# Optimization experiments

Hardware: AMD Instinct MI355X
Metric: run time of the kernel (lower is better)

The kernel has to match this reference:

```python
import jax, jax.numpy as jnp
import numpy as np

BATCH = 4096
DIM = 128
TEMP = 0.5
EPS = 1e-8


def _neg_mask(batch):
    n = 2 * batch
    m = np.ones((n, n), dtype=bool)
    np.fill_diagonal(m, False)
    idx = np.arange(batch)
    m[idx, idx + batch] = False
    m[idx + batch, idx] = False
    return m


def setup_inputs() -> dict:
    key = jax.random.key(0)
    k1, k2 = jax.random.split(key)
    zx = jax.random.normal(k1, (BATCH, DIM), dtype=jnp.float32)
    zy = jax.random.normal(k2, (BATCH, DIM), dtype=jnp.float32)
    return {"zx": zx, "zy": zy}


def reference(zx, zy):
    batch = zx.shape[0]
    n = 2 * batch  # N = 2 * batch_size
    z = jnp.concatenate([zx, zy], axis=0)  # [N, D]
    # cosine similarity = normalized GEMM (avoids O(N^2*D) intermediate)
    norm = jnp.maximum(jnp.linalg.norm(z, axis=1, keepdims=True), EPS)
    zn = z / norm
    sim = (zn @ zn.T) / TEMP  # [N, N]
    # positives: diagonals at offsets +batch and -batch
    sim_xy = jnp.diagonal(sim, offset=batch)
    sim_yx = jnp.diagonal(sim, offset=-batch)
    positives = jnp.concatenate([sim_xy, sim_yx]).reshape(n, 1)  # [N, 1]
    # negatives: mask out diagonal and positive pairs (static boolean mask)
    mask = _neg_mask(batch)
    negatives = sim[mask].reshape(n, n - 2)  # [N, N-2]
    logits = jnp.concatenate([positives, negatives], axis=1)  # [N, N-1]
    # CrossEntropy(labels=0, reduction='sum') / N
    loss = jnp.sum(jax.nn.logsumexp(logits, axis=1) - logits[:, 0]) / n
    return loss
```

## Files before the change

kernel.cpp:

```cpp
#include <hip/hip_runtime.h>
#include <hip/hip_bf16.h>

#define BATCH 4096
#define NROWS 8192
#define DIM   128

typedef __bf16 bf16x8 __attribute__((ext_vector_type(8)));
typedef __bf16 bf16x2 __attribute__((ext_vector_type(2)));
typedef float  f32x4  __attribute__((ext_vector_type(4)));

typedef const __attribute__((address_space(1))) unsigned int* gptr_t;
typedef __attribute__((address_space(3))) unsigned int* lptr_t;

__global__ __launch_bounds__(256) void normalize_kernel(
    const float* __restrict__ zx, const float* __restrict__ zy,
    ushort* __restrict__ zn)
{
  const int tid  = threadIdx.x;
  const int lane = tid & 63;
  const int w    = tid >> 6;
  const int row  = blockIdx.x * 4 + w;
  const float* src = (row < BATCH) ? (zx + (size_t)row * DIM)
                                   : (zy + (size_t)(row - BATCH) * DIM);
  float2 v = ((const float2*)src)[lane];
  float ss = v.x * v.x + v.y * v.y;
#pragma unroll
  for (int off = 1; off < 64; off <<= 1)
    ss += __shfl_xor(ss, off, 64);
  float inv = 1.0f / fmaxf(sqrtf(ss), 1e-8f);
  bf16x2 st;
  st.x = (__bf16)(v.x * inv);
  st.y = (__bf16)(v.y * inv);
  reinterpret_cast<bf16x2*>(zn + (size_t)row * DIM)[lane] = st;
}

__global__ __launch_bounds__(256, 2) void simloss_kernel(
    const ushort* __restrict__ zn, float* __restrict__ S, float* __restrict__ P)
{
  __shared__ ushort Bs[128 * 128];
  const int tid  = threadIdx.x;
  const int lane = tid & 63;
  const int w    = tid >> 6;
  const int wr   = w >> 1, wc = w & 1;
  const int rb    = blockIdx.x;
  const int strip = blockIdx.y;
  const int q    = lane >> 4;
  const int l15  = lane & 15;

  bf16x8 af[4][4];
  {
    const int arow = rb * 128 + wr * 64 + l15;
#pragma unroll
    for (int mi = 0; mi < 4; ++mi)
#pragma unroll
      for (int ks = 0; ks < 4; ++ks) {
        const ushort* ap = zn + (size_t)(arow + mi * 16) * DIM + ks * 32 + q * 8;
        af[mi][ks] = *reinterpret_cast<const bf16x8*>(ap);
      }
  }

  float Srow[4][4];
#pragma unroll
  for (int mi = 0; mi < 4; ++mi)
#pragma unroll
    for (int r = 0; r < 4; ++r) Srow[mi][r] = 0.f;

  const float K1 = 2.8853900817779268f;

  for (int it = 0; it < 8; ++it) {
    const int ct = strip * 8 + it;
    const int C0 = ct * 128;

    __syncthreads();
#pragma unroll
    for (int j = 0; j < 8; ++j) {
      const int Lbase = w * 512 + j * 64;
      const int row   = w * 32 + j * 4 + q;
      const int c     = l15 ^ (row & 15);
      const ushort* g = zn + (size_t)(C0 + row) * DIM + c * 8;
      __builtin_amdgcn_global_load_lds((gptr_t)g, (lptr_t)(Bs + Lbase * 8), 16, 0, 0);
    }
    __syncthreads();

    f32x4 acc[4][4];
#pragma unroll
    for (int mi = 0; mi < 4; ++mi)
#pragma unroll
      for (int ni = 0; ni < 4; ++ni)
        acc[mi][ni] = (f32x4){0.f, 0.f, 0.f, 0.f};

#pragma unroll
    for (int ks = 0; ks < 4; ++ks) {
      bf16x8 bf[4];
#pragma unroll
      for (int ni = 0; ni < 4; ++ni) {
        const int nl  = wc * 64 + ni * 16 + l15;
        const int ck  = ks * 4 + q;
        const int L   = nl * 16 + (ck ^ (nl & 15));
        bf[ni] = *reinterpret_cast<const bf16x8*>(Bs + L * 8);
      }
#pragma unroll
      for (int mi = 0; mi < 4; ++mi)
#pragma unroll
        for (int ni = 0; ni < 4; ++ni)
          acc[mi][ni] = __builtin_amdgcn_mfma_f32_16x16x32_bf16(
              af[mi][ks], bf[ni], acc[mi][ni], 0, 0, 0);
    }

    const bool diag = (ct == rb);
    const bool part = (ct == (rb ^ 32));
#pragma unroll
    for (int mi = 0; mi < 4; ++mi)
#pragma unroll
      for (int ni = 0; ni < 4; ++ni)
#pragma unroll
        for (int r = 0; r < 4; ++r) {
          float d = acc[mi][ni][r];
          float v = __builtin_amdgcn_exp2f(fmaf(d, K1, -K1));
          if (diag) {
            const int rl = wr * 64 + mi * 16 + q * 4 + r;
            const int cl = wc * 64 + ni * 16 + l15;
            if (rl == cl) v = 0.f;
          }
          Srow[mi][r] += v;
        }

    if (part) {
#pragma unroll
      for (int mi = 0; mi < 4; ++mi) {
        const int rl0 = wr * 64 + mi * 16 + q * 4;
#pragma unroll
        for (int ni = 0; ni < 4; ++ni) {
          const int cl = wc * 64 + ni * 16 + l15;
#pragma unroll
          for (int r = 0; r < 4; ++r) {
            if (cl == rl0 + r)
              P[rb * 128 + rl0 + r] = 2.0f * acc[mi][ni][r];
          }
        }
      }
    }
  }

#pragma unroll
  for (int mi = 0; mi < 4; ++mi)
#pragma unroll
    for (int r = 0; r < 4; ++r) {
      float v = Srow[mi][r];
      v += __shfl_xor(v, 1, 64);
      v += __shfl_xor(v, 2, 64);
      v += __shfl_xor(v, 4, 64);
      v += __shfl_xor(v, 8, 64);
      if (l15 == 0)
        atomicAdd(&S[rb * 128 + wr * 64 + mi * 16 + q * 4 + r], v);
    }
}

__global__ __launch_bounds__(256) void finalize_kernel(
    const float* __restrict__ S, const float* __restrict__ P,
    float* __restrict__ out)
{
  const int i = blockIdx.x * 256 + threadIdx.x;
  float c = 2.0f + logf(S[i]) - P[i];
#pragma unroll
  for (int off = 1; off < 64; off <<= 1)
    c += __shfl_xor(c, off, 64);
  __shared__ float wsum[4];
  const int lane = threadIdx.x & 63, w = threadIdx.x >> 6;
  if (lane == 0) wsum[w] = c;
  __syncthreads();
  if (threadIdx.x == 0)
    atomicAdd(out, (wsum[0] + wsum[1] + wsum[2] + wsum[3]) * (1.0f / NROWS));
}

extern "C" void kernel_launch(void* const* d_in, const int* in_sizes, int n_in,
                              void* d_out, int out_size, void* d_ws, size_t ws_size,
                              hipStream_t stream)
{
  const float* zx = (const float*)d_in[0];
  const float* zy = (const float*)d_in[1];
  ushort* zn = (ushort*)d_ws;
  float*  S  = (float*)((char*)d_ws + (size_t)NROWS * DIM * 2);
  float*  P  = S + NROWS;
  float*  out = (float*)d_out;

  hipMemsetAsync(S, 0, NROWS * sizeof(float), stream);
  hipMemsetAsync(out, 0, sizeof(float), stream);
  normalize_kernel<<<NROWS / 4, 256, 0, stream>>>(zx, zy, zn);
  simloss_kernel<<<dim3(64, 8), 256, 0, stream>>>(zn, S, P);
  finalize_kernel<<<NROWS / 256, 256, 0, stream>>>(S, P, out);
}
```

Measured before the change: 88.62 us.

## Double-buffer LDS B tiles and replace row-sum atomics with partial buffers

The similarity kernel now uses two LDS buffers for the B column tiles. It issues the async global-to-LDS load for the next tile before computing on the current one, so load latency overlaps the MFMA and exp work and one barrier per iteration goes away. Per-row exp sums are no longer accumulated with atomicAdd into a zeroed array. Each (strip, wave-column) writes its own partial-sum slice, and the finalize kernel adds the 16 slices per row, which also removes a memset. In exchange, LDS use per block doubles to 64KB and the workspace needs a larger partial-sum buffer.

```diff
diff --git a/kernel.cpp b/kernel.cpp
--- a/kernel.cpp
+++ b/kernel.cpp
@@ -35,9 +35,10 @@
 }
 
 __global__ __launch_bounds__(256, 2) void simloss_kernel(
-    const ushort* __restrict__ zn, float* __restrict__ S, float* __restrict__ P)
-{
-  __shared__ ushort Bs[128 * 128];
+    const ushort* __restrict__ zn, float* __restrict__ Spart,
+    float* __restrict__ P)
+{
+  __shared__ ushort Bs[2][128 * 128];
   const int tid  = threadIdx.x;
   const int lane = tid & 63;
   const int w    = tid >> 6;
@@ -47,6 +48,21 @@
   const int q    = lane >> 4;
   const int l15  = lane & 15;
 
+  auto stage = [&](int it, int buf) {
+    const int C0 = (strip * 8 + it) * 128;
+#pragma unroll
+    for (int j = 0; j < 8; ++j) {
+      const int Lbase = w * 512 + j * 64;
+      const int row   = w * 32 + j * 4 + q;
+      const int c     = l15 ^ (row & 15);
+      const ushort* g = zn + (size_t)(C0 + row) * DIM + c * 8;
+      __builtin_amdgcn_global_load_lds((gptr_t)g, (lptr_t)(&Bs[buf][Lbase * 8]),
+                                       16, 0, 0);
+    }
+  };
+
+  stage(0, 0);
+
   bf16x8 af[4][4];
   {
     const int arow = rb * 128 + wr * 64 + l15;
@@ -67,20 +83,15 @@
 
   const float K1 = 2.8853900817779268f;
 
+  __syncthreads();
+
   for (int it = 0; it < 8; ++it) {
-    const int ct = strip * 8 + it;
-    const int C0 = ct * 128;
-
-    __syncthreads();
-#pragma unroll
-    for (int j = 0; j < 8; ++j) {
-      const int Lbase = w * 512 + j * 64;
-      const int row   = w * 32 + j * 4 + q;
-      const int c     = l15 ^ (row & 15);
-      const ushort* g = zn + (size_t)(C0 + row) * DIM + c * 8;
-      __builtin_amdgcn_global_load_lds((gptr_t)g, (lptr_t)(Bs + Lbase * 8), 16, 0, 0);
-    }
-    __syncthreads();
+    const int cur = it & 1;
+    const int ct  = strip * 8 + it;
+
+    if (it < 7) stage(it + 1, cur ^ 1);
+
+    const ushort* bsc = &Bs[cur][0];
 
     f32x4 acc[4][4];
 #pragma unroll
@@ -97,7 +108,7 @@
         const int nl  = wc * 64 + ni * 16 + l15;
         const int ck  = ks * 4 + q;
         const int L   = nl * 16 + (ck ^ (nl & 15));
-        bf[ni] = *reinterpret_cast<const bf16x8*>(Bs + L * 8);
+        bf[ni] = *reinterpret_cast<const bf16x8*>(bsc + L * 8);
       }
 #pragma unroll
       for (int mi = 0; mi < 4; ++mi)
@@ -140,6 +151,8 @@
         }
       }
     }
+
+    if (it < 7) __syncthreads();
   }
 
 #pragma unroll
@@ -152,16 +165,20 @@
       v += __shfl_xor(v, 4, 64);
       v += __shfl_xor(v, 8, 64);
       if (l15 == 0)
-        atomicAdd(&S[rb * 128 + wr * 64 + mi * 16 + q * 4 + r], v);
+        Spart[(size_t)(strip * 2 + wc) * NROWS +
+              rb * 128 + wr * 64 + mi * 16 + q * 4 + r] = v;
     }
 }
 
 __global__ __launch_bounds__(256) void finalize_kernel(
-    const float* __restrict__ S, const float* __restrict__ P,
+    const float* __restrict__ Spart, const float* __restrict__ P,
     float* __restrict__ out)
 {
   const int i = blockIdx.x * 256 + threadIdx.x;
-  float c = 2.0f + logf(S[i]) - P[i];
+  float s = 0.f;
+#pragma unroll
+  for (int k = 0; k < 16; ++k) s += Spart[(size_t)k * NROWS + i];
+  float c = 2.0f + logf(s) - P[i];
 #pragma unroll
   for (int off = 1; off < 64; off <<= 1)
     c += __shfl_xor(c, off, 64);
@@ -180,13 +197,12 @@
   const float* zx = (const float*)d_in[0];
   const float* zy = (const float*)d_in[1];
   ushort* zn = (ushort*)d_ws;
-  float*  S  = (float*)((char*)d_ws + (size_t)NROWS * DIM * 2);
-  float*  P  = S + NROWS;
+  float*  P  = (float*)((char*)d_ws + (size_t)NROWS * DIM * 2);
+  float*  Sp = P + NROWS;
   float*  out = (float*)d_out;
 
-  hipMemsetAsync(S, 0, NROWS * sizeof(float), stream);
   hipMemsetAsync(out, 0, sizeof(float), stream);
   normalize_kernel<<<NROWS / 4, 256, 0, stream>>>(zx, zy, zn);
-  simloss_kernel<<<dim3(64, 8), 256, 0, stream>>>(zn, S, P);
-  finalize_kernel<<<NROWS / 256, 256, 0, stream>>>(S, P, out);
-}
+  simloss_kernel<<<dim3(64, 8), 256, 0, stream>>>(zn, Sp, P);
+  finalize_kernel<<<NROWS / 256, 256, 0, stream>>>(Sp, P, out);
+}
```

Measured after the change: 88.79 us. Within noise of the previous version (+0.2%).

## Exploit similarity symmetry: compute lower-triangular tiles with row and column exp-sums

Applied to the files above, without the earlier changes.

Each block now computes one lower-triangular 128x128 tile of the symmetric similarity matrix and adds exp values along both rows and columns. This roughly halves the MFMA and exp work. Per-tile partial sums go to a [64][8192] buffer that the finalize kernel adds up, which replaces the atomics and the memset. Each block now handles a single tile, so there is more launch and load overhead per tile, no reuse of the A fragment across tiles, and finalize reads extra memory.

```diff
diff --git a/kernel.cpp b/kernel.cpp
--- a/kernel.cpp
+++ b/kernel.cpp
@@ -1,9 +1,12 @@
 #include <hip/hip_runtime.h>
 #include <hip/hip_bf16.h>
+#include <math.h>
 
 #define BATCH 4096
 #define NROWS 8192
 #define DIM   128
+#define NTILE 64
+#define NBLK  (NTILE * (NTILE + 1) / 2)
 
 typedef __bf16 bf16x8 __attribute__((ext_vector_type(8)));
 typedef __bf16 bf16x2 __attribute__((ext_vector_type(2)));
@@ -35,43 +38,32 @@
 }
 
 __global__ __launch_bounds__(256, 2) void simloss_kernel(
-    const ushort* __restrict__ zn, float* __restrict__ S, float* __restrict__ P)
+    const ushort* __restrict__ zn, float* __restrict__ Spart,
+    float* __restrict__ P)
 {
   __shared__ ushort Bs[128 * 128];
   const int tid  = threadIdx.x;
   const int lane = tid & 63;
   const int w    = tid >> 6;
   const int wr   = w >> 1, wc = w & 1;
-  const int rb    = blockIdx.x;
-  const int strip = blockIdx.y;
   const int q    = lane >> 4;
   const int l15  = lane & 15;
 
-  bf16x8 af[4][4];
+  const int b = blockIdx.x;
+  int rb = 0;
   {
-    const int arow = rb * 128 + wr * 64 + l15;
-#pragma unroll
-    for (int mi = 0; mi < 4; ++mi)
-#pragma unroll
-      for (int ks = 0; ks < 4; ++ks) {
-        const ushort* ap = zn + (size_t)(arow + mi * 16) * DIM + ks * 32 + q * 8;
-        af[mi][ks] = *reinterpret_cast<const bf16x8*>(ap);
-      }
-  }
-
-  float Srow[4][4];
-#pragma unroll
-  for (int mi = 0; mi < 4; ++mi)
-#pragma unroll
-    for (int r = 0; r < 4; ++r) Srow[mi][r] = 0.f;
-
-  const float K1 = 2.8853900817779268f;
-
-  for (int it = 0; it < 8; ++it) {
-    const int ct = strip * 8 + it;
-    const int C0 = ct * 128;
-
-    __syncthreads();
+    int lo = 0, hi = NTILE - 1;
+    while (lo < hi) {
+      int mid = (lo + hi + 1) >> 1;
+      if (mid * (mid + 1) / 2 <= b) lo = mid; else hi = mid - 1;
+    }
+    rb = lo;
+  }
+  const int cb = b - rb * (rb + 1) / 2;
+  const bool diag = (rb == cb);
+
+  {
+    const int C0 = cb * 128;
 #pragma unroll
     for (int j = 0; j < 8; ++j) {
       const int Lbase = w * 512 + j * 64;
@@ -80,62 +72,88 @@
       const ushort* g = zn + (size_t)(C0 + row) * DIM + c * 8;
       __builtin_amdgcn_global_load_lds((gptr_t)g, (lptr_t)(Bs + Lbase * 8), 16, 0, 0);
     }
-    __syncthreads();
-
-    f32x4 acc[4][4];
+  }
+
+  bf16x8 af[4][4];
+  {
+    const int arow = rb * 128 + wr * 64 + l15;
 #pragma unroll
     for (int mi = 0; mi < 4; ++mi)
 #pragma unroll
+      for (int ks = 0; ks < 4; ++ks) {
+        const ushort* ap = zn + (size_t)(arow + mi * 16) * DIM + ks * 32 + q * 8;
+        af[mi][ks] = *reinterpret_cast<const bf16x8*>(ap);
+      }
+  }
+
+  __syncthreads();
+
+  f32x4 acc[4][4];
+#pragma unroll
+  for (int mi = 0; mi < 4; ++mi)
+#pragma unroll
+    for (int ni = 0; ni < 4; ++ni)
+      acc[mi][ni] = (f32x4){0.f, 0.f, 0.f, 0.f};
+
+#pragma unroll
+  for (int ks = 0; ks < 4; ++ks) {
+    bf16x8 bf[4];
+#pragma unroll
+    for (int ni = 0; ni < 4; ++ni) {
+      const int nl  = wc * 64 + ni * 16 + l15;
+      const int ck  = ks * 4 + q;
+      const int L   = nl * 16 + (ck ^ (nl & 15));
+      bf[ni] = *reinterpret_cast<const bf16x8*>(Bs + L * 8);
+    }
+#pragma unroll
+    for (int mi = 0; mi < 4; ++mi)
+#pragma unroll
       for (int ni = 0; ni < 4; ++ni)
-        acc[mi][ni] = (f32x4){0.f, 0.f, 0.f, 0.f};
-
-#pragma unroll
-    for (int ks = 0; ks < 4; ++ks) {
-      bf16x8 bf[4];
+        acc[mi][ni] = __builtin_amdgcn_mfma_f32_16x16x32_bf16(
+            af[mi][ks], bf[ni], acc[mi][ni], 0, 0, 0);
+  }
+
+  const float K1 = 2.8853900817779268f;
+  float Srow[4][4];
+  float Scol[4];
+#pragma unroll
+  for (int mi = 0; mi < 4; ++mi)
+#pragma unroll
+    for (int r = 0; r < 4; ++r) Srow[mi][r] = 0.f;
+#pragma unroll
+  for (int ni = 0; ni < 4; ++ni) Scol[ni] = 0.f;
+
+#pragma unroll
+  for (int mi = 0; mi < 4; ++mi)
+#pragma unroll
+    for (int ni = 0; ni < 4; ++ni)
+#pragma unroll
+      for (int r = 0; r < 4; ++r) {
+        float d = acc[mi][ni][r];
+        float v = __builtin_amdgcn_exp2f(fmaf(d, K1, -K1));
+        if (diag) {
+          const int rl = wr * 64 + mi * 16 + q * 4 + r;
+          const int cl = wc * 64 + ni * 16 + l15;
+          if (rl == cl) v = 0.f;
+        }
+        Srow[mi][r] += v;
+        Scol[ni]    += v;
+      }
+
+  if (rb >= 32 && cb == rb - 32) {
+#pragma unroll
+    for (int mi = 0; mi < 4; ++mi) {
+      const int rl0 = wr * 64 + mi * 16 + q * 4;
 #pragma unroll
       for (int ni = 0; ni < 4; ++ni) {
-        const int nl  = wc * 64 + ni * 16 + l15;
-        const int ck  = ks * 4 + q;
-        const int L   = nl * 16 + (ck ^ (nl & 15));
-        bf[ni] = *reinterpret_cast<const bf16x8*>(Bs + L * 8);
-      }
-#pragma unroll
-      for (int mi = 0; mi < 4; ++mi)
-#pragma unroll
-        for (int ni = 0; ni < 4; ++ni)
-          acc[mi][ni] = __builtin_amdgcn_mfma_f32_16x16x32_bf16(
-              af[mi][ks], bf[ni], acc[mi][ni], 0, 0, 0);
-    }
-
-    const bool diag = (ct == rb);
-    const bool part = (ct == (rb ^ 32));
-#pragma unroll
-    for (int mi = 0; mi < 4; ++mi)
-#pragma unroll
-      for (int ni = 0; ni < 4; ++ni)
+        const int cl = wc * 64 + ni * 16 + l15;
 #pragma unroll
         for (int r = 0; r < 4; ++r) {
-          float d = acc[mi][ni][r];
-          float v = __builtin_amdgcn_exp2f(fmaf(d, K1, -K1));
-          if (diag) {
-            const int rl = wr * 64 + mi * 16 + q * 4 + r;
-            const int cl = wc * 64 + ni * 16 + l15;
-            if (rl == cl) v = 0.f;
-          }
-          Srow[mi][r] += v;
-        }
-
-    if (part) {
-#pragma unroll
-      for (int mi = 0; mi < 4; ++mi) {
-        const int rl0 = wr * 64 + mi * 16 + q * 4;
-#pragma unroll
-        for (int ni = 0; ni < 4; ++ni) {
-          const int cl = wc * 64 + ni * 16 + l15;
-#pragma unroll
-          for (int r = 0; r < 4; ++r) {
-            if (cl == rl0 + r)
-              P[rb * 128 + rl0 + r] = 2.0f * acc[mi][ni][r];
+          if (cl == rl0 + r) {
+            const int gr = rb * 128 + rl0 + r;
+            const float pv = 2.0f * acc[mi][ni][r];
+            P[gr] = pv;
+            P[gr - 4096] = pv;
           }
         }
       }
@@ -151,17 +169,49 @@
       v += __shfl_xor(v, 2, 64);
       v += __shfl_xor(v, 4, 64);
       v += __shfl_xor(v, 8, 64);
-      if (l15 == 0)
-        atomicAdd(&S[rb * 128 + wr * 64 + mi * 16 + q * 4 + r], v);
-    }
+      Srow[mi][r] = v;
+    }
+#pragma unroll
+  for (int ni = 0; ni < 4; ++ni) {
+    float v = Scol[ni];
+    v += __shfl_xor(v, 16, 64);
+    v += __shfl_xor(v, 32, 64);
+    Scol[ni] = v;
+  }
+
+  __syncthreads();
+  float* sc = (float*)Bs;
+  if (l15 == 0) {
+#pragma unroll
+    for (int mi = 0; mi < 4; ++mi)
+#pragma unroll
+      for (int r = 0; r < 4; ++r)
+        sc[wc * 128 + wr * 64 + mi * 16 + q * 4 + r] = Srow[mi][r];
+  }
+  if (lane < 16) {
+#pragma unroll
+    for (int ni = 0; ni < 4; ++ni)
+      sc[256 + wr * 128 + wc * 64 + ni * 16 + l15] = Scol[ni];
+  }
+  __syncthreads();
+
+  if (tid < 128) {
+    Spart[(size_t)cb * NROWS + rb * 128 + tid] = sc[tid] + sc[128 + tid];
+  } else if (!diag) {
+    const int c = tid - 128;
+    Spart[(size_t)rb * NROWS + cb * 128 + c] = sc[256 + c] + sc[384 + c];
+  }
 }
 
 __global__ __launch_bounds__(256) void finalize_kernel(
-    const float* __restrict__ S, const float* __restrict__ P,
+    const float* __restrict__ Spart, const float* __restrict__ P,
     float* __restrict__ out)
 {
   const int i = blockIdx.x * 256 + threadIdx.x;
-  float c = 2.0f + logf(S[i]) - P[i];
+  float s = 0.f;
+#pragma unroll 16
+  for (int k = 0; k < NTILE; ++k) s += Spart[(size_t)k * NROWS + i];
+  float c = 2.0f + logf(s) - P[i];
 #pragma unroll
   for (int off = 1; off < 64; off <<= 1)
     c += __shfl_xor(c, off, 64);
@@ -180,13 +230,12 @@
   const float* zx = (const float*)d_in[0];
   const float* zy = (const float*)d_in[1];
   ushort* zn = (ushort*)d_ws;
-  float*  S  = (float*)((char*)d_ws + (size_t)NROWS * DIM * 2);
-  float*  P  = S + NROWS;
+  float*  P  = (float*)((char*)d_ws + (size_t)NROWS * DIM * 2);
+  float*  Sp = P + NROWS;
   float*  out = (float*)d_out;
 
-  hipMemsetAsync(S, 0, NROWS * sizeof(float), stream);
   hipMemsetAsync(out, 0, sizeof(float), stream);
   normalize_kernel<<<NROWS / 4, 256, 0, stream>>>(zx, zy, zn);
-  simloss_kernel<<<dim3(64, 8), 256, 0, stream>>>(zn, S, P);
-  finalize_kernel<<<NROWS / 256, 256, 0, stream>>>(S, P, out);
-}
+  simloss_kernel<<<NBLK, 256, 0, stream>>>(zn, Sp, P);
+  finalize_kernel<<<NROWS / 256, 256, 0, stream>>>(Sp, P, out);
+}
```

Result: no change. 89.59 us (+1.1%).

## Exploit symmetry of similarity matrix with triangular tiles and double-buffered B loads

Applied to the files above, without the earlier changes.

Computes only the lower-triangular 128x128 tiles of the symmetric similarity matrix. Each off-diagonal tile contributes its exp-sum to both row and column sums through column-reduction atomics. The 2080 tiles are spread over 512 blocks by pairing triangle rows p and 63-p, and the B-tile loads into LDS are double-buffered to overlap with MFMA work. The S zeroing memset is folded into the normalize kernel. This roughly halves the GEMM and exp work, at the cost of more atomics, double the LDS, and some load imbalance.

```diff
diff --git a/kernel.cpp b/kernel.cpp
--- a/kernel.cpp
+++ b/kernel.cpp
@@ -4,6 +4,7 @@
 #define BATCH 4096
 #define NROWS 8192
 #define DIM   128
+#define NTILE 64
 
 typedef __bf16 bf16x8 __attribute__((ext_vector_type(8)));
 typedef __bf16 bf16x2 __attribute__((ext_vector_type(2)));
@@ -14,12 +15,13 @@
 
 __global__ __launch_bounds__(256) void normalize_kernel(
     const float* __restrict__ zx, const float* __restrict__ zy,
-    ushort* __restrict__ zn)
+    ushort* __restrict__ zn, float* __restrict__ S)
 {
   const int tid  = threadIdx.x;
   const int lane = tid & 63;
   const int w    = tid >> 6;
   const int row  = blockIdx.x * 4 + w;
+  if (blockIdx.x < 32) S[blockIdx.x * 256 + tid] = 0.f;
   const float* src = (row < BATCH) ? (zx + (size_t)row * DIM)
                                    : (zy + (size_t)(row - BATCH) * DIM);
   float2 v = ((const float2*)src)[lane];
@@ -35,52 +37,79 @@
 }
 
 __global__ __launch_bounds__(256, 2) void simloss_kernel(
-    const ushort* __restrict__ zn, float* __restrict__ S, float* __restrict__ P)
-{
-  __shared__ ushort Bs[128 * 128];
+    const ushort* __restrict__ zn, float* __restrict__ S,
+    float* __restrict__ P)
+{
+  __shared__ ushort Bs[2][128 * 128];
   const int tid  = threadIdx.x;
   const int lane = tid & 63;
   const int w    = tid >> 6;
   const int wr   = w >> 1, wc = w & 1;
-  const int rb    = blockIdx.x;
-  const int strip = blockIdx.y;
   const int q    = lane >> 4;
   const int l15  = lane & 15;
 
-  bf16x8 af[4][4];
-  {
-    const int arow = rb * 128 + wr * 64 + l15;
-#pragma unroll
-    for (int mi = 0; mi < 4; ++mi)
-#pragma unroll
-      for (int ks = 0; ks < 4; ++ks) {
-        const ushort* ap = zn + (size_t)(arow + mi * 16) * DIM + ks * 32 + q * 8;
-        af[mi][ks] = *reinterpret_cast<const bf16x8*>(ap);
-      }
-  }
-
-  float Srow[4][4];
-#pragma unroll
-  for (int mi = 0; mi < 4; ++mi)
-#pragma unroll
-    for (int r = 0; r < 4; ++r) Srow[mi][r] = 0.f;
-
-  const float K1 = 2.8853900817779268f;
-
-  for (int it = 0; it < 8; ++it) {
-    const int ct = strip * 8 + it;
-    const int C0 = ct * 128;
-
-    __syncthreads();
+  const int p  = blockIdx.x >> 4;
+  const int ch = blockIdx.x & 15;
+  const int o0 = (ch == 0) ? 0 : 1 + ch * 4;
+  const int T  = (ch == 0) ? 5 : 4;
+  const int L0 = p + 1;
+
+  auto tile_rc = [&](int o, int& rb, int& cb) {
+    if (o < L0) { rb = p;      cb = o; }
+    else        { rb = 63 - p; cb = o - L0; }
+  };
+
+  auto stage = [&](int cb, int buf) {
+    const int C0 = cb * 128;
 #pragma unroll
     for (int j = 0; j < 8; ++j) {
       const int Lbase = w * 512 + j * 64;
       const int row   = w * 32 + j * 4 + q;
       const int c     = l15 ^ (row & 15);
       const ushort* g = zn + (size_t)(C0 + row) * DIM + c * 8;
-      __builtin_amdgcn_global_load_lds((gptr_t)g, (lptr_t)(Bs + Lbase * 8), 16, 0, 0);
-    }
-    __syncthreads();
+      __builtin_amdgcn_global_load_lds((gptr_t)g, (lptr_t)(&Bs[buf][Lbase * 8]),
+                                       16, 0, 0);
+    }
+  };
+
+  bf16x8 af[4][4];
+  auto loadA = [&](int rb) {
+    const int arow = rb * 128 + wr * 64 + l15;
+#pragma unroll
+    for (int mi = 0; mi < 4; ++mi)
+#pragma unroll
+      for (int ks = 0; ks < 4; ++ks) {
+        const ushort* ap = zn + (size_t)(arow + mi * 16) * DIM + ks * 32 + q * 8;
+        af[mi][ks] = *reinterpret_cast<const bf16x8*>(ap);
+      }
+  };
+
+  int rb0, cb0;
+  tile_rc(o0, rb0, cb0);
+  stage(cb0, 0);
+  loadA(rb0);
+
+  float Srow[4][4];
+#pragma unroll
+  for (int mi = 0; mi < 4; ++mi)
+#pragma unroll
+    for (int r = 0; r < 4; ++r) Srow[mi][r] = 0.f;
+
+  const float K1 = 2.8853900817779268f;
+
+  __syncthreads();
+
+  for (int t = 0; t < T; ++t) {
+    const int o = o0 + t;
+    int trb, tcb;
+    tile_rc(o, trb, tcb);
+    int nrb = -1, ncb = -1;
+    if (t + 1 < T) {
+      tile_rc(o + 1, nrb, ncb);
+      stage(ncb, (t & 1) ^ 1);
+    }
+
+    const ushort* bsc = &Bs[t & 1][0];
 
     f32x4 acc[4][4];
 #pragma unroll
@@ -97,7 +126,7 @@
         const int nl  = wc * 64 + ni * 16 + l15;
         const int ck  = ks * 4 + q;
         const int L   = nl * 16 + (ck ^ (nl & 15));
-        bf[ni] = *reinterpret_cast<const bf16x8*>(Bs + L * 8);
+        bf[ni] = *reinterpret_cast<const bf16x8*>(bsc + L * 8);
       }
 #pragma unroll
       for (int mi = 0; mi < 4; ++mi)
@@ -107,8 +136,11 @@
               af[mi][ks], bf[ni], acc[mi][ni], 0, 0, 0);
     }
 
-    const bool diag = (ct == rb);
-    const bool part = (ct == (rb ^ 32));
+    const bool diag = (trb == tcb);
+    float Scol[4];
+#pragma unroll
+    for (int ni = 0; ni < 4; ++ni) Scol[ni] = 0.f;
+
 #pragma unroll
     for (int mi = 0; mi < 4; ++mi)
 #pragma unroll
@@ -123,9 +155,10 @@
             if (rl == cl) v = 0.f;
           }
           Srow[mi][r] += v;
+          Scol[ni]    += v;
         }
 
-    if (part) {
+    if (trb - tcb == 32) {
 #pragma unroll
       for (int mi = 0; mi < 4; ++mi) {
         const int rl0 = wr * 64 + mi * 16 + q * 4;
@@ -134,26 +167,50 @@
           const int cl = wc * 64 + ni * 16 + l15;
 #pragma unroll
           for (int r = 0; r < 4; ++r) {
-            if (cl == rl0 + r)
-              P[rb * 128 + rl0 + r] = 2.0f * acc[mi][ni][r];
+            if (cl == rl0 + r) {
+              const int gr = trb * 128 + rl0 + r;
+              const float pv = 2.0f * acc[mi][ni][r];
+              P[gr] = pv;
+              P[gr - 4096] = pv;
+            }
           }
         }
       }
     }
+
+    if (!diag) {
+#pragma unroll
+      for (int ni = 0; ni < 4; ++ni) {
+        float v = Scol[ni];
+        v += __shfl_xor(v, 16, 64);
+        v += __shfl_xor(v, 32, 64);
+        if (lane < 16)
+          atomicAdd(&S[tcb * 128 + wc * 64 + ni * 16 + l15], v);
+      }
+    }
+
+    const bool flushR = (t == T - 1) || (nrb != trb);
+    if (flushR) {
+#pragma unroll
+      for (int mi = 0; mi < 4; ++mi)
+#pragma unroll
+        for (int r = 0; r < 4; ++r) {
+          float v = Srow[mi][r];
+          v += __shfl_xor(v, 1, 64);
+          v += __shfl_xor(v, 2, 64);
+          v += __shfl_xor(v, 4, 64);
+          v += __shfl_xor(v, 8, 64);
+          if (l15 == 0)
+            atomicAdd(&S[trb * 128 + wr * 64 + mi * 16 + q * 4 + r], v);
+          Srow[mi][r] = 0.f;
+        }
+    }
+
+    if (t + 1 < T) {
+      if (nrb != trb) loadA(nrb);
+      __syncthreads();
+    }
   }
-
-#pragma unroll
-  for (int mi = 0; mi < 4; ++mi)
-#pragma unroll
-    for (int r = 0; r < 4; ++r) {
-      float v = Srow[mi][r];
-      v += __shfl_xor(v, 1, 64);
-      v += __shfl_xor(v, 2, 64);
-      v += __shfl_xor(v, 4, 64);
-      v += __shfl_xor(v, 8, 64);
-      if (l15 == 0)
-        atomicAdd(&S[rb * 128 + wr * 64 + mi * 16 + q * 4 + r], v);
-    }
 }
 
 __global__ __launch_bounds__(256) void finalize_kernel(
@@ -180,13 +237,12 @@
   const float* zx = (const float*)d_in[0];
   const float* zy = (const float*)d_in[1];
   ushort* zn = (ushort*)d_ws;
-  float*  S  = (float*)((char*)d_ws + (size_t)NROWS * DIM * 2);
-  float*  P  = S + NROWS;
+  float*  P  = (float*)((char*)d_ws + (size_t)NROWS * DIM * 2);
+  float*  S  = P + NROWS;
   float*  out = (float*)d_out;
 
-  hipMemsetAsync(S, 0, NROWS * sizeof(float), stream);
   hipMemsetAsync(out, 0, sizeof(float), stream);
-  normalize_kernel<<<NROWS / 4, 256, 0, stream>>>(zx, zy, zn);
-  simloss_kernel<<<dim3(64, 8), 256, 0, stream>>>(zn, S, P);
+  normalize_kernel<<<NROWS / 4, 256, 0, stream>>>(zx, zy, zn, S);
+  simloss_kernel<<<512, 256, 0, stream>>>(zn, S, P);
   finalize_kernel<<<NROWS / 256, 256, 0, stream>>>(S, P, out);
 }
```

Measured after the change: 86.40 us. 1.03x faster.
